# Performance work log

Hardware: AMD Instinct MI355X
Metric: run time of the kernel (lower is better)

Reference implementation:

```python
import jax, jax.numpy as jnp
import numpy as np

EMB = 16
L = 100
B = 8192
BN_EPS = 1e-5


def _bn(x, g, b):
    # BatchNorm1d in training mode: biased batch stats over dim 0. x: [b, EMB]
    mu = jnp.mean(x, axis=0)
    var = jnp.mean((x - mu) ** 2, axis=0)
    return g * (x - mu) / jnp.sqrt(var + BN_EPS) + b


def _pool(me, aw, g6, b6, a6):
    # me: [b, L, EMB] masked embeddings; aw: [b, L, 1] masked attention logits
    s = jnp.sum(me, axis=1)                       # sum pool
    mean = jnp.mean(me, axis=1)                   # mean over full L (incl. padding), as in torch
    sq = me * me
    l2 = jnp.sum(sq, axis=-1)                     # [b, L]
    mx_i = jnp.argmax(l2, axis=1)                 # first max, matches torch.max
    mn_i = jnp.argmin(jnp.where(l2 == 0, jnp.asarray(9999.0, l2.dtype), l2), axis=1)
    mx = jnp.take_along_axis(me, mx_i[:, None, None], axis=1)[:, 0]
    mn = jnp.take_along_axis(me, mn_i[:, None, None], axis=1)[:, 0]
    attw = jax.nn.softmax(aw, axis=1)             # softmax over L incl. zeroed pads (faithful)
    at = jnp.sum(me * attw, axis=1)
    ko = 0.5 * (s * s - jnp.sum(sq, axis=1))      # korder (FM-style)
    ko = ko / jnp.maximum(jnp.linalg.norm(ko, axis=-1, keepdims=True), 1e-12)
    # branch order: sum, mean, max, min, korder, atten (matches torch.cat order)
    pools = jnp.stack([
        _bn(s, g6[0], b6[0]), _bn(mean, g6[1], b6[1]), _bn(mx, g6[2], b6[2]),
        _bn(mn, g6[3], b6[3]), _bn(ko, g6[4], b6[4]), _bn(at, g6[5], b6[5])], axis=1)
    w = jax.nn.softmax(a6)[None, :, None]
    return jnp.sum(pools * w, axis=1)             # [b, EMB]


def setup_inputs() -> dict:
    key = jax.random.key(0)
    ks = jax.random.split(key, 24)
    f32 = jnp.float32
    inp = {
        'uid': jax.random.randint(ks[0], (B,), 0, 139000),
        'mid': jax.random.randint(ks[1], (B,), 0, 132000),
        'yr': jax.random.randint(ks[2], (B,), 0, 150),
        'ids_ug': jax.random.randint(ks[3], (B, L), 0, 30),
        'ids_urb': jax.random.randint(ks[4], (B, L), 0, 132000),
        'ids_mg': jax.random.randint(ks[5], (B, L), 0, 30),
        'ids_mt': jax.random.randint(ks[6], (B, L), 0, 41000),
        'len_ug': jax.random.randint(ks[7], (B,), 1, L + 1),
        'len_urb': jax.random.randint(ks[8], (B,), 1, L + 1),
        'len_mg': jax.random.randint(ks[9], (B,), 1, L + 1),
        'len_mt': jax.random.randint(ks[10], (B,), 1, L + 1),
        'emb_userId': jax.random.normal(ks[11], (139000, EMB), f32) * 0.05,
        'emb_movieId': jax.random.normal(ks[12], (132000, EMB), f32) * 0.05,
        'emb_tagId': jax.random.normal(ks[13], (41000, EMB), f32) * 0.05,
        'emb_genreId': jax.random.normal(ks[14], (30, EMB), f32) * 0.05,
        'emb_year': jax.random.normal(ks[15], (150, EMB), f32) * 0.05,
        # init_param(): atten embeddings ~ N(1.0, 1e-6)
        'att_movieId': 1.0 + jax.random.normal(ks[16], (132000, 1), f32) * 1e-6,
        'att_tagId': 1.0 + jax.random.normal(ks[17], (41000, 1), f32) * 1e-6,
        'att_genreId': 1.0 + jax.random.normal(ks[18], (30, 1), f32) * 1e-6,
        'bn_gamma': jnp.ones((4, 6, EMB), f32),
        'bn_beta': jnp.zeros((4, 6, EMB), f32),
        'alpha': jnp.ones((4, 6), f32),
        'W1': jax.random.normal(ks[19], (112, 64), f32) * 0.05,
        'b1': jnp.zeros((64,), f32),
        'W2': jax.random.normal(ks[20], (64, 32), f32) * 0.05,
        'b2': jnp.zeros((32,), f32),
        'W3': jax.random.normal(ks[21], (32, 1), f32) * 0.05,
        'b3': jnp.zeros((1,), f32),
    }
    return inp


def reference(uid, mid, yr, ids_ug, ids_urb, ids_mg, ids_mt,
              len_ug, len_urb, len_mg, len_mt,
              emb_userId, emb_movieId, emb_tagId, emb_genreId, emb_year,
              att_movieId, att_tagId, att_genreId,
              bn_gamma, bn_beta, alpha, W1, b1, W2, b2, W3, b3):
    emb1 = jnp.concatenate([emb_userId[uid], emb_movieId[mid], emb_year[yr]], axis=1)  # [b, 48]
    ar = jnp.arange(L)
    fields = [
        (ids_ug, len_ug, emb_genreId, att_genreId),
        (ids_urb, len_urb, emb_movieId, att_movieId),
        (ids_mg, len_mg, emb_genreId, att_genreId),
        (ids_mt, len_mt, emb_tagId, att_tagId),
    ]
    pooled = []
    for i, (ids, ln, tab, atab) in enumerate(fields):
        m = (ln[:, None] > ar)[..., None].astype(tab.dtype)  # [b, L, 1]
        me = tab[ids] * m
        aw = atab[ids] * m
        pooled.append(_pool(me, aw, bn_gamma[i], bn_beta[i], alpha[i]))
    x = jnp.concatenate([emb1] + pooled, axis=1)  # [b, 112]
    h = jax.nn.relu(x @ W1 + b1)
    h = jax.nn.relu(h @ W2 + b2)
    return jax.nn.sigmoid(h @ W3 + b3)[:, 0]
```

## Files before the change

### kernel.cpp

```cpp
#include <hip/hip_runtime.h>
#include <math.h>

#define BATCH 8192
#define L 100
#define EMB 16
#define NCH 384
#define NG  512

#define POOLED_FLOATS (4 * BATCH * 96)
#define POOLED_BYTES  (POOLED_FLOATS * 4)
#define PART_FLOATS   (NCH * NG)

__global__ __launch_bounds__(256) void pool_kernel(
    const int* __restrict__ ids_ug, const int* __restrict__ ids_urb,
    const int* __restrict__ ids_mg, const int* __restrict__ ids_mt,
    const int* __restrict__ len_ug, const int* __restrict__ len_urb,
    const int* __restrict__ len_mg, const int* __restrict__ len_mt,
    const float* __restrict__ emb_movie, const float* __restrict__ emb_tag,
    const float* __restrict__ emb_genre,
    const float* __restrict__ att_movie, const float* __restrict__ att_tag,
    const float* __restrict__ att_genre,
    float* __restrict__ pooled, float* __restrict__ psum, float* __restrict__ psq)
{
    const int bx  = blockIdx.x;
    const int f   = bx & 3;
    const int g   = bx >> 2;
    const int tid = threadIdx.x;
    const int sub = tid >> 4;
    const int e   = tid & 15;
    const int j   = e >> 2;
    const int c   = e & 3;
    const int b   = g * 16 + sub;

    const int* ids; const int* lens; const float* tab; const float* atab;
    switch (f) {
        case 0: ids = ids_ug;  lens = len_ug;  tab = emb_genre; atab = att_genre; break;
        case 1: ids = ids_urb; lens = len_urb; tab = emb_movie; atab = att_movie; break;
        case 2: ids = ids_mg;  lens = len_mg;  tab = emb_genre; atab = att_genre; break;
        default:ids = ids_mt;  lens = len_mt;  tab = emb_tag;   atab = att_tag;   break;
    }
    const int ln = lens[b];
    const float4* __restrict__ tab4 = (const float4*)tab;

    __shared__ float tile[16][100];
    __shared__ int   sids[16 * 100];
    __shared__ float gtab[480];
    __shared__ float gexp[32];

    {
        const int4* idsrc = (const int4*)(ids + (size_t)g * (16 * L));
        ((int4*)sids)[tid]       = idsrc[tid];
        if (tid < 144) ((int4*)sids)[256 + tid] = idsrc[256 + tid];
    }
    const bool genre = (f == 0) | (f == 2);
    if (genre) {
        for (int i = tid; i < 480; i += 256) gtab[i] = emb_genre[i];
        if (tid < 30) gexp[tid] = __expf(att_genre[tid]);
    }
    __syncthreads();
    const int* idrow = &sids[sub * 100];

    float4 s   = make_float4(0.f, 0.f, 0.f, 0.f);
    float4 ssq = s, att = s, mxv = s, mnv = s;
    float expsum = 0.f;
    float bestmx = -1e30f; int lx = 0x7fffffff;
    float bestmn =  1e30f; int lm = 0x7fffffff;

    auto ACC = [&](const float4 v, const float ew, const int l) {
        float4 v2;
        v2.x = v.x * v.x; v2.y = v.y * v.y; v2.z = v.z * v.z; v2.w = v.w * v.w;
        s.x += v.x; s.y += v.y; s.z += v.z; s.w += v.w;
        ssq.x += v2.x; ssq.y += v2.y; ssq.z += v2.z; ssq.w += v2.w;
        float pl2 = (v2.x + v2.y) + (v2.z + v2.w);
        float l2 = pl2 + __shfl_xor(pl2, 1);
        l2 += __shfl_xor(l2, 2);
        if (l2 > bestmx) { bestmx = l2; lx = l; mxv = v; }
        float l2m = (l2 == 0.0f) ? 9999.0f : l2;
        if (l2m < bestmn) { bestmn = l2m; lm = l; mnv = v; }
        expsum += ew;
        att.x += v.x * ew; att.y += v.y * ew; att.z += v.z * ew; att.w += v.w * ew;
    };

    if (!genre) {
        int l = j;
        if (l < ln) {
            int id0 = idrow[l];
            float4 v0 = tab4[(size_t)id0 * 4 + c];
            float aw0 = atab[id0];
            while (l + 4 < ln) {
                const int id1 = idrow[l + 4];
                float4 v1 = tab4[(size_t)id1 * 4 + c];
                float aw1 = atab[id1];
                ACC(v0, __expf(aw0), l);
                v0 = v1; aw0 = aw1; l += 4;
            }
            ACC(v0, __expf(aw0), l);
        }
    } else {
        for (int l = j; l < ln; l += 4) {
            const int id = idrow[l];
            float4 v = *(const float4*)&gtab[id * 16 + c * 4];
            ACC(v, gexp[id], l);
        }
    }

    #pragma unroll
    for (int m = 4; m <= 8; m <<= 1) {
        float obx = __shfl_xor(bestmx, m);
        int   olx = __shfl_xor(lx, m);
        float ax = __shfl_xor(mxv.x, m), ay = __shfl_xor(mxv.y, m);
        float az = __shfl_xor(mxv.z, m), aw2 = __shfl_xor(mxv.w, m);
        if (obx > bestmx || (obx == bestmx && olx < lx)) {
            bestmx = obx; lx = olx; mxv = make_float4(ax, ay, az, aw2);
        }
        float obn = __shfl_xor(bestmn, m);
        int   olm = __shfl_xor(lm, m);
        float bx2 = __shfl_xor(mnv.x, m), by = __shfl_xor(mnv.y, m);
        float bz  = __shfl_xor(mnv.z, m), bw = __shfl_xor(mnv.w, m);
        if (obn < bestmn || (obn == bestmn && olm < lm)) {
            bestmn = obn; lm = olm; mnv = make_float4(bx2, by, bz, bw);
        }
        s.x += __shfl_xor(s.x, m); s.y += __shfl_xor(s.y, m);
        s.z += __shfl_xor(s.z, m); s.w += __shfl_xor(s.w, m);
        ssq.x += __shfl_xor(ssq.x, m); ssq.y += __shfl_xor(ssq.y, m);
        ssq.z += __shfl_xor(ssq.z, m); ssq.w += __shfl_xor(ssq.w, m);
        att.x += __shfl_xor(att.x, m); att.y += __shfl_xor(att.y, m);
        att.z += __shfl_xor(att.z, m); att.w += __shfl_xor(att.w, m);
        expsum += __shfl_xor(expsum, m);
    }
    expsum += (float)(L - ln);

    float4 mean;
    mean.x = s.x * (1.0f / L); mean.y = s.y * (1.0f / L);
    mean.z = s.z * (1.0f / L); mean.w = s.w * (1.0f / L);
    float4 ko;
    ko.x = 0.5f * (s.x * s.x - ssq.x); ko.y = 0.5f * (s.y * s.y - ssq.y);
    ko.z = 0.5f * (s.z * s.z - ssq.z); ko.w = 0.5f * (s.w * s.w - ssq.w);
    float pk = (ko.x * ko.x + ko.y * ko.y) + (ko.z * ko.z + ko.w * ko.w);
    float kn2 = pk + __shfl_xor(pk, 1);
    kn2 += __shfl_xor(kn2, 2);
    float rn = 1.0f / fmaxf(sqrtf(kn2), 1e-12f);
    ko.x *= rn; ko.y *= rn; ko.z *= rn; ko.w *= rn;
    float ie = 1.0f / expsum;
    att.x *= ie; att.y *= ie; att.z *= ie; att.w *= ie;

    float4 pv[6] = { s, mean, mxv, mnv, ko, att };

    float4* prow = (float4*)(pooled + ((size_t)(f * BATCH + b)) * 96);
    if (j == 0) {
        #pragma unroll
        for (int p = 0; p < 6; ++p) {
            prow[p * 4 + c] = pv[p];
            *(float4*)&tile[sub][p * 16 + c * 4] = pv[p];
        }
    }
    __syncthreads();
    if (tid < 96) {
        float sm = 0.f, sq = 0.f;
        #pragma unroll
        for (int s2 = 0; s2 < 16; ++s2) {
            float x = tile[s2][tid];
            sm += x;
            sq += x * x;
        }
        psum[(size_t)(f * 96 + tid) * NG + g] = sm;
        psq [(size_t)(f * 96 + tid) * NG + g] = sq;
    }
}

__global__ __launch_bounds__(256) void coef_kernel(
    const float* __restrict__ psum, const float* __restrict__ psq,
    const float* __restrict__ gamma, const float* __restrict__ beta,
    const float* __restrict__ alpha,
    float* __restrict__ coefA, float* __restrict__ coefB)
{
    const int tid   = threadIdx.x;
    const int chl   = tid >> 3;
    const int strip = tid & 7;
    const int ch    = blockIdx.x * 32 + chl;
    const float4* ps = (const float4*)(psum + (size_t)ch * NG + strip * 64);
    const float4* pq = (const float4*)(psq  + (size_t)ch * NG + strip * 64);
    double dsm = 0.0, dsq = 0.0;
    #pragma unroll
    for (int i = 0; i < 16; ++i) {
        float4 a = ps[i];
        dsm += ((double)a.x + (double)a.y) + ((double)a.z + (double)a.w);
        float4 bq = pq[i];
        dsq += ((double)bq.x + (double)bq.y) + ((double)bq.z + (double)bq.w);
    }
    #pragma unroll
    for (int m = 1; m <= 4; m <<= 1) {
        dsm += __shfl_xor(dsm, m);
        dsq += __shfl_xor(dsq, m);
    }
    if (strip == 0) {
        const int f = ch / 96;
        const int p = (ch % 96) >> 4;
        double mu  = dsm * (1.0 / BATCH);
        double var = dsq * (1.0 / BATCH) - mu * mu;
        float inv = (float)(1.0 / sqrt(var + 1e-5));
        float gm = gamma[ch];
        float bb = beta[ch];
        float amax = -1e30f;
        for (int q = 0; q < 6; ++q) amax = fmaxf(amax, alpha[f * 6 + q]);
        float wsum = 0.f;
        for (int q = 0; q < 6; ++q) wsum += __expf(alpha[f * 6 + q] - amax);
        float wp = __expf(alpha[f * 6 + p] - amax) / wsum;
        coefA[ch] = wp * gm * inv;
        coefB[ch] = wp * (bb - gm * (float)mu * inv);
    }
}

#define SPB 16
__global__ __launch_bounds__(256) void final_kernel(
    const int* __restrict__ uid, const int* __restrict__ mid, const int* __restrict__ yr,
    const float* __restrict__ emb_user, const float* __restrict__ emb_movie,
    const float* __restrict__ emb_year,
    const float* __restrict__ pooled,
    const float* __restrict__ coefA, const float* __restrict__ coefB,
    const float* __restrict__ W1, const float* __restrict__ b1,
    const float* __restrict__ W2, const float* __restrict__ b2,
    const float* __restrict__ W3, const float* __restrict__ b3,
    float* __restrict__ out)
{
    __shared__ float sW1[112 * 64];
    __shared__ float sW2[64 * 32];
    __shared__ float sW3[32];
    __shared__ float sb1[64];
    __shared__ float sb2[32];
    __shared__ float xt[SPB][112];
    __shared__ float h1t[SPB][64];

    const int tid = threadIdx.x;
    for (int i = tid; i < 112 * 16; i += 256)
        ((float4*)sW1)[i] = ((const float4*)W1)[i];
    for (int i = tid; i < 64 * 8; i += 256)
        ((float4*)sW2)[i] = ((const float4*)W2)[i];
    if (tid < 32) sW3[tid] = W3[tid];
    if (tid < 64) sb1[tid] = b1[tid];
    if (tid < 32) sb2[tid] = b2[tid];

    const int sub = tid >> 4;
    const int e   = tid & 15;
    const int b   = blockIdx.x * SPB + sub;

    xt[sub][e]      = emb_user [(size_t)uid[b] * EMB + e];
    xt[sub][16 + e] = emb_movie[(size_t)mid[b] * EMB + e];
    xt[sub][32 + e] = emb_year [(size_t)yr[b]  * EMB + e];

    #pragma unroll
    for (int f = 0; f < 4; ++f) {
        const float* pr = pooled + ((size_t)(f * BATCH + b)) * 96;
        float acc = 0.f;
        #pragma unroll
        for (int p = 0; p < 6; ++p) {
            int c = f * 96 + p * 16 + e;
            acc += coefA[c] * pr[p * 16 + e] + coefB[c];
        }
        xt[sub][48 + f * 16 + e] = acc;
    }
    __syncthreads();

    float4 h1 = ((float4*)sb1)[e];
    for (int k = 0; k < 112; ++k) {
        float xk = xt[sub][k];
        float4 w = ((float4*)sW1)[k * 16 + e];
        h1.x += xk * w.x; h1.y += xk * w.y; h1.z += xk * w.z; h1.w += xk * w.w;
    }
    float4 h1r;
    h1r.x = fmaxf(h1.x, 0.f); h1r.y = fmaxf(h1.y, 0.f);
    h1r.z = fmaxf(h1.z, 0.f); h1r.w = fmaxf(h1.w, 0.f);
    *(float4*)&h1t[sub][e * 4] = h1r;
    __syncthreads();

    float2 h2 = ((float2*)sb2)[e];
    for (int k = 0; k < 64; ++k) {
        float hk = h1t[sub][k];
        float2 w = ((float2*)sW2)[k * 16 + e];
        h2.x += hk * w.x; h2.y += hk * w.y;
    }
    float part = fmaxf(h2.x, 0.f) * sW3[2 * e] + fmaxf(h2.y, 0.f) * sW3[2 * e + 1];
    part += __shfl_xor(part, 1);
    part += __shfl_xor(part, 2);
    part += __shfl_xor(part, 4);
    part += __shfl_xor(part, 8);
    if (e == 0) {
        float t = part + b3[0];
        out[b] = 1.f / (1.f + __expf(-t));
    }
}

extern "C" void kernel_launch(void* const* d_in, const int* in_sizes, int n_in,
                              void* d_out, int out_size, void* d_ws, size_t ws_size,
                              hipStream_t stream) {
    const int* uid     = (const int*)d_in[0];
    const int* mid     = (const int*)d_in[1];
    const int* yr      = (const int*)d_in[2];
    const int* ids_ug  = (const int*)d_in[3];
    const int* ids_urb = (const int*)d_in[4];
    const int* ids_mg  = (const int*)d_in[5];
    const int* ids_mt  = (const int*)d_in[6];
    const int* len_ug  = (const int*)d_in[7];
    const int* len_urb = (const int*)d_in[8];
    const int* len_mg  = (const int*)d_in[9];
    const int* len_mt  = (const int*)d_in[10];
    const float* emb_user  = (const float*)d_in[11];
    const float* emb_movie = (const float*)d_in[12];
    const float* emb_tag   = (const float*)d_in[13];
    const float* emb_genre = (const float*)d_in[14];
    const float* emb_year  = (const float*)d_in[15];
    const float* att_movie = (const float*)d_in[16];
    const float* att_tag   = (const float*)d_in[17];
    const float* att_genre = (const float*)d_in[18];
    const float* bn_gamma  = (const float*)d_in[19];
    const float* bn_beta   = (const float*)d_in[20];
    const float* alpha     = (const float*)d_in[21];
    const float* W1 = (const float*)d_in[22];
    const float* b1 = (const float*)d_in[23];
    const float* W2 = (const float*)d_in[24];
    const float* b2 = (const float*)d_in[25];
    const float* W3 = (const float*)d_in[26];
    const float* b3 = (const float*)d_in[27];
    float* out = (float*)d_out;

    float* pooled = (float*)d_ws;
    float* psum   = pooled + POOLED_FLOATS;
    float* psq    = psum + PART_FLOATS;
    float* coefA  = psq + PART_FLOATS;
    float* coefB  = coefA + NCH;

    pool_kernel<<<4 * NG, 256, 0, stream>>>(
        ids_ug, ids_urb, ids_mg, ids_mt,
        len_ug, len_urb, len_mg, len_mt,
        emb_movie, emb_tag, emb_genre,
        att_movie, att_tag, att_genre,
        pooled, psum, psq);
    coef_kernel<<<12, 256, 0, stream>>>(psum, psq, bn_gamma, bn_beta, alpha,
                                        coefA, coefB);
    final_kernel<<<BATCH / SPB, 256, 0, stream>>>(
        uid, mid, yr, emb_user, emb_movie, emb_year,
        pooled, coefA, coefB, W1, b1, W2, b2, W3, b3, out);
}
```

Before: 168.5 us.

## Pack movie/tag tables to bf16 rows with fused attention logit and L2

Adds a pre-pass kernel that repacks the movie and tag embedding tables each call into 64-byte records. Each record holds the bf16-rounded embedding, the fp32 attention logit and a precomputed fp32 squared norm. The pool kernel then gathers one record per id and spreads the fields across lanes with shuffles. This is meant to remove the separate attention-table gather and the per-element L2 shuffle reduction. In exchange it adds a full read of both tables and a write of the packed copy on every call, and it lowers embedding precision to bf16.

```diff
diff --git a/kernel.cpp b/kernel.cpp
--- a/kernel.cpp
+++ b/kernel.cpp
@@ -6,20 +6,60 @@
 #define EMB 16
 #define NCH 384
 #define NG  512
+#define N_MOVIE 132000
+#define N_TAG   41000
 
 #define POOLED_FLOATS (4 * BATCH * 96)
-#define POOLED_BYTES  (POOLED_FLOATS * 4)
 #define PART_FLOATS   (NCH * NG)
+#define WS_HDR_FLOATS (POOLED_FLOATS + 2 * PART_FLOATS + 2 * NCH)
+
+__device__ __forceinline__ unsigned bf16rne(float x) {
+    unsigned u = __float_as_uint(x);
+    return (u + 0x7fffu + ((u >> 16) & 1u)) >> 16;
+}
+__device__ __forceinline__ unsigned pack2(float a, float b) {
+    return bf16rne(a) | (bf16rne(b) << 16);
+}
+
+__global__ __launch_bounds__(256) void pack_kernel(
+    const float* __restrict__ emb_movie, const float* __restrict__ att_movie,
+    const float* __restrict__ emb_tag,   const float* __restrict__ att_tag,
+    uint4* __restrict__ pk_movie, uint4* __restrict__ pk_tag)
+{
+    int i = blockIdx.x * 256 + threadIdx.x;
+    const float* src; float a; uint4* dst;
+    if (i < N_MOVIE) {
+        src = emb_movie + (size_t)i * 16; a = att_movie[i];
+        dst = pk_movie + (size_t)i * 4;
+    } else {
+        i -= N_MOVIE;
+        if (i >= N_TAG) return;
+        src = emb_tag + (size_t)i * 16; a = att_tag[i];
+        dst = pk_tag + (size_t)i * 4;
+    }
+    const float4* s4 = (const float4*)src;
+    float4 r0 = s4[0], r1 = s4[1], r2 = s4[2], r3 = s4[3];
+    float l2 = ((r0.x*r0.x + r0.y*r0.y) + (r0.z*r0.z + r0.w*r0.w))
+             + ((r1.x*r1.x + r1.y*r1.y) + (r1.z*r1.z + r1.w*r1.w))
+             + ((r2.x*r2.x + r2.y*r2.y) + (r2.z*r2.z + r2.w*r2.w))
+             + ((r3.x*r3.x + r3.y*r3.y) + (r3.z*r3.z + r3.w*r3.w));
+    uint4 q0, q1, q2;
+    q0.x = pack2(r0.x, r0.y); q0.y = pack2(r0.z, r0.w);
+    q0.z = pack2(r1.x, r1.y); q0.w = pack2(r1.z, r1.w);
+    q1.x = pack2(r2.x, r2.y); q1.y = pack2(r2.z, r2.w);
+    q1.z = pack2(r3.x, r3.y); q1.w = pack2(r3.z, r3.w);
+    q2.x = __float_as_uint(a); q2.y = __float_as_uint(l2);
+    q2.z = 0u; q2.w = 0u;
+    dst[0] = q0; dst[1] = q1; dst[2] = q2;
+}
 
 __global__ __launch_bounds__(256) void pool_kernel(
     const int* __restrict__ ids_ug, const int* __restrict__ ids_urb,
     const int* __restrict__ ids_mg, const int* __restrict__ ids_mt,
     const int* __restrict__ len_ug, const int* __restrict__ len_urb,
     const int* __restrict__ len_mg, const int* __restrict__ len_mt,
-    const float* __restrict__ emb_movie, const float* __restrict__ emb_tag,
-    const float* __restrict__ emb_genre,
-    const float* __restrict__ att_movie, const float* __restrict__ att_tag,
-    const float* __restrict__ att_genre,
+    const uint4* __restrict__ pk_movie, const uint4* __restrict__ pk_tag,
+    const float* __restrict__ emb_genre, const float* __restrict__ att_genre,
     float* __restrict__ pooled, float* __restrict__ psum, float* __restrict__ psq)
 {
     const int bx  = blockIdx.x;
@@ -31,16 +71,16 @@
     const int j   = e >> 2;
     const int c   = e & 3;
     const int b   = g * 16 + sub;
-
-    const int* ids; const int* lens; const float* tab; const float* atab;
+    const int qb  = (tid & 63) & ~3;
+
+    const int* ids; const int* lens; const uint4* pk;
     switch (f) {
-        case 0: ids = ids_ug;  lens = len_ug;  tab = emb_genre; atab = att_genre; break;
-        case 1: ids = ids_urb; lens = len_urb; tab = emb_movie; atab = att_movie; break;
-        case 2: ids = ids_mg;  lens = len_mg;  tab = emb_genre; atab = att_genre; break;
-        default:ids = ids_mt;  lens = len_mt;  tab = emb_tag;   atab = att_tag;   break;
+        case 0: ids = ids_ug;  lens = len_ug;  pk = 0;         break;
+        case 1: ids = ids_urb; lens = len_urb; pk = pk_movie;  break;
+        case 2: ids = ids_mg;  lens = len_mg;  pk = 0;         break;
+        default:ids = ids_mt;  lens = len_mt;  pk = pk_tag;    break;
     }
     const int ln = lens[b];
-    const float4* __restrict__ tab4 = (const float4*)tab;
 
     __shared__ float tile[16][100];
     __shared__ int   sids[16 * 100];
@@ -49,7 +89,7 @@
 
     {
         const int4* idsrc = (const int4*)(ids + (size_t)g * (16 * L));
-        ((int4*)sids)[tid]       = idsrc[tid];
+        ((int4*)sids)[tid] = idsrc[tid];
         if (tid < 144) ((int4*)sids)[256 + tid] = idsrc[256 + tid];
     }
     const bool genre = (f == 0) | (f == 2);
@@ -66,41 +106,53 @@
     float bestmx = -1e30f; int lx = 0x7fffffff;
     float bestmn =  1e30f; int lm = 0x7fffffff;
 
-    auto ACC = [&](const float4 v, const float ew, const int l) {
-        float4 v2;
-        v2.x = v.x * v.x; v2.y = v.y * v.y; v2.z = v.z * v.z; v2.w = v.w * v.w;
+    auto ACCV = [&](const float4 v, const float l2v, const float ew, const int l) {
         s.x += v.x; s.y += v.y; s.z += v.z; s.w += v.w;
-        ssq.x += v2.x; ssq.y += v2.y; ssq.z += v2.z; ssq.w += v2.w;
-        float pl2 = (v2.x + v2.y) + (v2.z + v2.w);
-        float l2 = pl2 + __shfl_xor(pl2, 1);
-        l2 += __shfl_xor(l2, 2);
-        if (l2 > bestmx) { bestmx = l2; lx = l; mxv = v; }
-        float l2m = (l2 == 0.0f) ? 9999.0f : l2;
+        ssq.x += v.x * v.x; ssq.y += v.y * v.y;
+        ssq.z += v.z * v.z; ssq.w += v.w * v.w;
+        if (l2v > bestmx) { bestmx = l2v; lx = l; mxv = v; }
+        float l2m = (l2v == 0.0f) ? 9999.0f : l2v;
         if (l2m < bestmn) { bestmn = l2m; lm = l; mnv = v; }
         expsum += ew;
         att.x += v.x * ew; att.y += v.y * ew; att.z += v.z * ew; att.w += v.w * ew;
     };
 
     if (!genre) {
+        auto ACCP = [&](const uint4 q, const int l) {
+            float aw  = __uint_as_float(__shfl((int)q.x, qb + 2, 64));
+            float l2v = __uint_as_float(__shfl((int)q.y, qb + 2, 64));
+            const int rs = qb + (c >> 1);
+            unsigned wa = (unsigned)__shfl((int)q.x, rs, 64);
+            unsigned wb = (unsigned)__shfl((int)q.y, rs, 64);
+            unsigned wc = (unsigned)__shfl((int)q.z, rs, 64);
+            unsigned wd = (unsigned)__shfl((int)q.w, rs, 64);
+            const unsigned u0 = (c & 1) ? wc : wa;
+            const unsigned u1 = (c & 1) ? wd : wb;
+            float4 v;
+            v.x = __uint_as_float(u0 << 16);
+            v.y = __uint_as_float(u0 & 0xffff0000u);
+            v.z = __uint_as_float(u1 << 16);
+            v.w = __uint_as_float(u1 & 0xffff0000u);
+            ACCV(v, l2v, __expf(aw), l);
+        };
         int l = j;
         if (l < ln) {
-            int id0 = idrow[l];
-            float4 v0 = tab4[(size_t)id0 * 4 + c];
-            float aw0 = atab[id0];
+            uint4 q0 = pk[(size_t)idrow[l] * 4 + c];
             while (l + 4 < ln) {
-                const int id1 = idrow[l + 4];
-                float4 v1 = tab4[(size_t)id1 * 4 + c];
-                float aw1 = atab[id1];
-                ACC(v0, __expf(aw0), l);
-                v0 = v1; aw0 = aw1; l += 4;
+                uint4 q1 = pk[(size_t)idrow[l + 4] * 4 + c];
+                ACCP(q0, l);
+                q0 = q1; l += 4;
             }
-            ACC(v0, __expf(aw0), l);
+            ACCP(q0, l);
         }
     } else {
         for (int l = j; l < ln; l += 4) {
             const int id = idrow[l];
             float4 v = *(const float4*)&gtab[id * 16 + c * 4];
-            ACC(v, gexp[id], l);
+            float pl2 = (v.x * v.x + v.y * v.y) + (v.z * v.z + v.w * v.w);
+            float l2v = pl2 + __shfl_xor(pl2, 1);
+            l2v += __shfl_xor(l2v, 2);
+            ACCV(v, l2v, gexp[id], l);
         }
     }
 
@@ -136,8 +188,8 @@
     float4 ko;
     ko.x = 0.5f * (s.x * s.x - ssq.x); ko.y = 0.5f * (s.y * s.y - ssq.y);
     ko.z = 0.5f * (s.z * s.z - ssq.z); ko.w = 0.5f * (s.w * s.w - ssq.w);
-    float pk = (ko.x * ko.x + ko.y * ko.y) + (ko.z * ko.z + ko.w * ko.w);
-    float kn2 = pk + __shfl_xor(pk, 1);
+    float pk2 = (ko.x * ko.x + ko.y * ko.y) + (ko.z * ko.z + ko.w * ko.w);
+    float kn2 = pk2 + __shfl_xor(pk2, 1);
     kn2 += __shfl_xor(kn2, 2);
     float rn = 1.0f / fmaxf(sqrtf(kn2), 1e-12f);
     ko.x *= rn; ko.y *= rn; ko.z *= rn; ko.w *= rn;
@@ -328,12 +380,15 @@
     float* psq    = psum + PART_FLOATS;
     float* coefA  = psq + PART_FLOATS;
     float* coefB  = coefA + NCH;
-
+    uint4* pk_movie = (uint4*)((char*)d_ws + (size_t)WS_HDR_FLOATS * 4);
+    uint4* pk_tag   = pk_movie + (size_t)N_MOVIE * 4;
+
+    pack_kernel<<<(N_MOVIE + N_TAG + 255) / 256, 256, 0, stream>>>(
+        emb_movie, att_movie, emb_tag, att_tag, pk_movie, pk_tag);
     pool_kernel<<<4 * NG, 256, 0, stream>>>(
         ids_ug, ids_urb, ids_mg, ids_mt,
         len_ug, len_urb, len_mg, len_mt,
-        emb_movie, emb_tag, emb_genre,
-        att_movie, att_tag, att_genre,
+        pk_movie, pk_tag, emb_genre, att_genre,
         pooled, psum, psq);
     coef_kernel<<<12, 256, 0, stream>>>(psum, psq, bn_gamma, bn_beta, alpha,
                                         coefA, coefB);
```

New measurement: 172.6 us. +2.4%, slower.
